# Kernel tuning notes

Measured on AMD Instinct MI355X. Metric: run time of the kernel, lower is better.

The kernel has to match this reference:

```python
import jax, jax.numpy as jnp
import numpy as np

DN = ('NCDHW', 'OIDHW', 'NCDHW')
HEADS, DIM_HEAD = 8, 64
BN_EPS = 1e-5


def conv3d(x, w, stride=1, padding=0, groups=1):
    return jax.lax.conv_general_dilated(
        x, w, window_strides=(stride,) * 3,
        padding=[(padding, padding)] * 3,
        feature_group_count=groups, dimension_numbers=DN)


def batchnorm(x, g, b, m, v):
    sh = (1, -1, 1, 1, 1)
    return (x - m.reshape(sh)) * jax.lax.rsqrt(v.reshape(sh) + BN_EPS) * g.reshape(sh) + b.reshape(sh)


def setup_inputs() -> dict:
    key = jax.random.key(0)
    ks = jax.random.split(key, 6)
    dim, inner = 128, HEADS * DIM_HEAD
    inp = {
        'x': jax.random.normal(ks[0], (4, dim, 16, 16, 16), jnp.float32),
        'wq_dw': jax.random.normal(ks[1], (dim, 1, 3, 3, 3), jnp.float32) * 0.1,
        'bn_q_g': jnp.ones((dim,), jnp.float32),
        'bn_q_b': jnp.zeros((dim,), jnp.float32),
        'bn_q_m': jnp.zeros((dim,), jnp.float32),
        'bn_q_v': jnp.ones((dim,), jnp.float32),
        'wq_pw': jax.random.normal(ks[2], (inner, dim, 1, 1, 1), jnp.float32) * 0.05,
        'wkv_dw': jax.random.normal(ks[3], (dim, 1, 3, 3, 3), jnp.float32) * 0.1,
        'bn_kv_g': jnp.ones((dim,), jnp.float32),
        'bn_kv_b': jnp.zeros((dim,), jnp.float32),
        'bn_kv_m': jnp.zeros((dim,), jnp.float32),
        'bn_kv_v': jnp.ones((dim,), jnp.float32),
        'wkv_pw': jax.random.normal(ks[4], (2 * inner, dim, 1, 1, 1), jnp.float32) * 0.05,
        'w_out': jax.random.normal(ks[5], (dim, inner, 1, 1, 1), jnp.float32) * 0.05,
        'b_out': jnp.zeros((dim,), jnp.float32),
    }
    return inp


def reference(x, wq_dw, bn_q_g, bn_q_b, bn_q_m, bn_q_v, wq_pw,
              wkv_dw, bn_kv_g, bn_kv_b, bn_kv_m, bn_kv_v, wkv_pw,
              w_out, b_out):
    b, c, z, xx, y = x.shape
    h, d = HEADS, DIM_HEAD
    inner = h * d
    scale = d ** -0.5

    # Q projection: depthwise conv (stride 1) -> BN (eval) -> pointwise conv
    q = conv3d(x, wq_dw, stride=1, padding=1, groups=c)
    q = batchnorm(q, bn_q_g, bn_q_b, bn_q_m, bn_q_v)
    q = conv3d(q, wq_pw)                      # [b, inner, z, x, y]

    # KV projection: depthwise conv (stride 2) -> BN -> pointwise conv
    kv = conv3d(x, wkv_dw, stride=2, padding=1, groups=c)
    kv = batchnorm(kv, bn_kv_g, bn_kv_b, bn_kv_m, bn_kv_v)
    kv = conv3d(kv, wkv_pw)                   # [b, 2*inner, z/2, x/2, y/2]
    k, v = kv[:, :inner], kv[:, inner:]

    nq = z * xx * y
    nk = k.shape[2] * k.shape[3] * k.shape[4]
    # channels split as (h d): reshape to [b, h, d, n]
    q4 = q.reshape(b, h, d, nq)
    k4 = k.reshape(b, h, d, nk)
    v4 = v.reshape(b, h, d, nk)

    dots = jnp.einsum('bhdi,bhdj->bhij', q4, k4) * scale   # [b,h,nq,nk]
    attn = jax.nn.softmax(dots, axis=-1)
    out = jnp.einsum('bhij,bhdj->bhdi', attn, v4)          # [b,h,d,nq]
    out = out.reshape(b, inner, z, xx, y)

    out = conv3d(out, w_out) + b_out.reshape(1, -1, 1, 1, 1)
    return out
```

## Files before the change

kernel.cpp:

```cpp
#include <hip/hip_runtime.h>
#include <hip/hip_bf16.h>

typedef __attribute__((ext_vector_type(8))) short short8;
typedef __attribute__((ext_vector_type(4))) short short4v;
typedef __attribute__((ext_vector_type(4))) float f32x4;

#define MFMA16(a, b, c) __builtin_amdgcn_mfma_f32_16x16x32_bf16((a), (b), (c), 0, 0, 0)


__device__ __forceinline__ short f2bf(float f) {
    union { __hip_bfloat16 h; short s; } u;
    u.h = __float2bfloat16(f);
    return u.s;
}

__device__ __forceinline__ unsigned pk2(float lo, float hi) {
    unsigned a = (unsigned short)f2bf(lo);
    unsigned b = (unsigned short)f2bf(hi);
    return a | (b << 16);
}

#define C2SCALE 0.18033688011112042f

__global__ __launch_bounds__(256) void dw_kernel(
    const float* __restrict__ x,
    const float* __restrict__ wq_dw, const float* __restrict__ qg, const float* __restrict__ qb,
    const float* __restrict__ qm, const float* __restrict__ qv,
    const float* __restrict__ wkv_dw, const float* __restrict__ kg, const float* __restrict__ kb,
    const float* __restrict__ km, const float* __restrict__ kv,
    const float* __restrict__ wq_pw, const float* __restrict__ wkv_pw, const float* __restrict__ wo,
    short* __restrict__ qd_t, short* __restrict__ kvd_t,
    short* __restrict__ wq_bf, short* __restrict__ wkv_bf, short* __restrict__ wo_bf) {
    __shared__ float xs[16][3][16][17];
    const int cg = blockIdx.x, by = blockIdx.y, b = blockIdx.z;
    const int tid = threadIdx.x;

    if (by == 24) {
        const int base = (b * 8 + cg) * 256 + tid;
        for (int i = base; i < 65536; i += 8192) {
            int o = i >> 7, cin = i & 127;
            wq_bf[((o >> 4) * 4 + (cin >> 5)) * 512 + (((cin >> 3) & 3) * 16 + (o & 15)) * 8 + (cin & 7)] = f2bf(wq_pw[i]);
        }
        for (int i = base; i < 131072; i += 8192) {
            int o = i >> 7, cin = i & 127;
            wkv_bf[((o >> 4) * 4 + (cin >> 5)) * 512 + (((cin >> 3) & 3) * 16 + (o & 15)) * 8 + (cin & 7)] = f2bf(wkv_pw[i]);
        }
        for (int i = base; i < 65536; i += 8192) {
            int o = i >> 9, cin = i & 511;
            wo_bf[((o >> 4) * 16 + (cin >> 5)) * 512 + (((cin >> 3) & 3) * 16 + (o & 15)) * 8 + (cin & 7)] = f2bf(wo[i]);
        }
        return;
    }

    const int y = tid >> 4, xx = tid & 15;
    const int c0 = cg * 16;

    if (by < 16) {
        const int z = by;
        #pragma unroll 4
        for (int ch = 0; ch < 16; ++ch)
            for (int zz = 0; zz < 3; ++zz) {
                int iz = z + zz - 1;
                float val = 0.f;
                if ((unsigned)iz < 16u)
                    val = x[(((b * 128 + c0 + ch) * 16 + iz) * 16 + y) * 16 + xx];
                xs[ch][zz][y][xx] = val;
            }
        __syncthreads();
        short res[16];
        #pragma unroll
        for (int ch = 0; ch < 16; ++ch) {
            const int c = c0 + ch;
            const float* wc = wq_dw + c * 27;
            float s = 0.f;
            #pragma unroll
            for (int zz = 0; zz < 3; ++zz)
                #pragma unroll
                for (int dy = 0; dy < 3; ++dy) {
                    int iy = y + dy - 1;
                    if ((unsigned)iy < 16u) {
                        float v  = xs[ch][zz][iy][xx];
                        float vm = __shfl_up(v, 1, 16);
                        float vp = __shfl_down(v, 1, 16);
                        float w0 = wc[zz * 9 + dy * 3 + 0];
                        float w1 = wc[zz * 9 + dy * 3 + 1];
                        float w2 = wc[zz * 9 + dy * 3 + 2];
                        if (xx > 0)  s += vm * w0;
                        s += v * w1;
                        if (xx < 15) s += vp * w2;
                    }
                }
            float sc = qg[c] * rsqrtf(qv[c] + 1e-5f);
            float sh = qb[c] - qm[c] * sc;
            res[ch] = f2bf(s * sc + sh);
        }
        const int i = z * 256 + tid;
        const int ib = i >> 4;
        short* dstb = qd_t + (long)b * 524288;
        #pragma unroll
        for (int h2 = 0; h2 < 2; ++h2) {
            short8 ov;
            #pragma unroll
            for (int k = 0; k < 8; ++k) ov[k] = res[h2 * 8 + k];
            *(short8*)(dstb + (ib * 4 + (cg >> 1)) * 512 + (((cg * 2 + h2) & 3) * 16 + xx) * 8) = ov;
        }
    } else {
        const int oz = by - 16;
        #pragma unroll 4
        for (int ch = 0; ch < 16; ++ch)
            for (int zz = 0; zz < 3; ++zz) {
                int iz = 2 * oz + zz - 1;
                float val = 0.f;
                if ((unsigned)iz < 16u)
                    val = x[(((b * 128 + c0 + ch) * 16 + iz) * 16 + y) * 16 + xx];
                xs[ch][zz][y][xx] = val;
            }
        __syncthreads();
        const int pos = tid & 63, cq = tid >> 6;
        const int oy = pos >> 3, ox = pos & 7;
        short4v outv;
        #pragma unroll
        for (int cc = 0; cc < 4; ++cc) {
            const int chl = cq * 4 + cc;
            const int c = c0 + chl;
            const float* wc = wkv_dw + c * 27;
            float s = 0.f;
            #pragma unroll
            for (int zz = 0; zz < 3; ++zz)
                #pragma unroll
                for (int dy = 0; dy < 3; ++dy) {
                    int iy = 2 * oy + dy - 1;
                    if ((unsigned)iy < 16u) {
                        #pragma unroll
                        for (int dx = 0; dx < 3; ++dx) {
                            int ix = 2 * ox + dx - 1;
                            if ((unsigned)ix < 16u)
                                s += xs[chl][zz][iy][ix] * wc[zz * 9 + dy * 3 + dx];
                        }
                    }
                }
            float sc = kg[c] * rsqrtf(kv[c] + 1e-5f);
            float sh = kb[c] - km[c] * sc;
            outv[cc] = f2bf(s * sc + sh);
        }
        const int j = oz * 64 + pos;
        const int jb = j >> 4;
        short* dstb = kvd_t + (long)b * 65536;
        *(short4v*)(dstb + (jb * 4 + (cg >> 1)) * 512 +
                    (((cg * 2 + (cq >> 1)) & 3) * 16 + (j & 15)) * 8 + (cq & 1) * 4) = outv;
    }
}

__global__ __launch_bounds__(256) void pw_kernel(
    const short* __restrict__ wq_bf, const short* __restrict__ wkv_bf,
    const short* __restrict__ qd_t, const short* __restrict__ kvd_t,
    short* __restrict__ q_t, short* __restrict__ k_t, short* __restrict__ v_t) {
    const int xid = blockIdx.x, b = blockIdx.y;
    const int tid = threadIdx.x, lane = tid & 63, wv = tid >> 6;
    const int jl = lane & 15, gq = lane >> 4;
    const int wm = wv >> 1, wn = wv & 1;

    if (xid < 128) {
        const int bi = xid >> 2, bo = xid & 3;
        short8 A[4][4];
        #pragma unroll
        for (int m = 0; m < 4; ++m)
            #pragma unroll
            for (int ks = 0; ks < 4; ++ks)
                A[m][ks] = *(const short8*)(wq_bf + (((bo * 8 + wm * 4 + m) * 4 + ks) * 512) + lane * 8);
        f32x4 acc[4][4];
        #pragma unroll
        for (int m = 0; m < 4; ++m)
            #pragma unroll
            for (int n = 0; n < 4; ++n) acc[m][n] = (f32x4){0.f, 0.f, 0.f, 0.f};
        const short* Bb = qd_t + (long)b * 524288;
        #pragma unroll
        for (int ks = 0; ks < 4; ++ks)
            #pragma unroll
            for (int n = 0; n < 4; ++n) {
                short8 Bf = *(const short8*)(Bb + (((bi * 8 + wn * 4 + n) * 4 + ks) * 512) + lane * 8);
                #pragma unroll
                for (int m = 0; m < 4; ++m) acc[m][n] = MFMA16(A[m][ks], Bf, acc[m][n]);
            }
        const int h = bo * 2 + wm;
        short* qf = q_t + ((long)(b * 8 + h)) * 262144;
        #pragma unroll
        for (int m = 0; m < 4; ++m)
            #pragma unroll
            for (int n = 0; n < 4; ++n) {
                int it = bi * 8 + wn * 4 + n;
                short4v pk;
                #pragma unroll
                for (int r = 0; r < 4; ++r) pk[r] = f2bf(acc[m][n][r] * C2SCALE);
                *(short4v*)(qf + (it * 2 + (m >> 1)) * 512 +
                            (((m & 1) * 2 + (gq >> 1)) * 16 + jl) * 8 + (gq & 1) * 4) = pk;
            }
    } else {
        const int e = xid - 128;
        const int bj = e >> 3, bo = e & 7;
        short8 A[4][4];
        #pragma unroll
        for (int m = 0; m < 4; ++m)
            #pragma unroll
            for (int ks = 0; ks < 4; ++ks)
                A[m][ks] = *(const short8*)(wkv_bf + (((bo * 8 + wm * 4 + m) * 4 + ks) * 512) + lane * 8);
        f32x4 acc[4][4];
        #pragma unroll
        for (int m = 0; m < 4; ++m)
            #pragma unroll
            for (int n = 0; n < 4; ++n) acc[m][n] = (f32x4){0.f, 0.f, 0.f, 0.f};
        const short* Bb = kvd_t + (long)b * 65536;
        #pragma unroll
        for (int ks = 0; ks < 4; ++ks)
            #pragma unroll
            for (int n = 0; n < 4; ++n) {
                short8 Bf = *(const short8*)(Bb + (((bj * 8 + wn * 4 + n) * 4 + ks) * 512) + lane * 8);
                #pragma unroll
                for (int m = 0; m < 4; ++m) acc[m][n] = MFMA16(A[m][ks], Bf, acc[m][n]);
            }
        const int hh = bo * 2 + wm;
        if (hh < 8) {
            short* kf = k_t + ((long)(b * 8 + hh)) * 32768;
            #pragma unroll
            for (int m = 0; m < 4; ++m)
                #pragma unroll
                for (int n = 0; n < 4; ++n) {
                    int jb16 = bj * 8 + wn * 4 + n;
                    short4v pk;
                    #pragma unroll
                    for (int r = 0; r < 4; ++r) pk[r] = f2bf(acc[m][n][r]);
                    *(short4v*)(kf + (jb16 * 2 + (m >> 1)) * 512 +
                                (((m & 1) * 2 + (gq >> 1)) * 16 + jl) * 8 + (gq & 1) * 4) = pk;
                }
        } else {
            short* vf = v_t + ((long)(b * 8 + hh - 8)) * 32768;
            #pragma unroll
            for (int m = 0; m < 4; ++m)
                #pragma unroll
                for (int n = 0; n < 4; ++n) {
                    int frag = ((bj * 4 + wn * 2 + (n >> 1)) * 4 + m);
                    #pragma unroll
                    for (int r = 0; r < 4; ++r)
                        vf[frag * 512 + ((jl >> 2) * 16 + gq * 4 + r) * 8 + (n & 1) * 4 + (jl & 3)]
                            = f2bf(acc[m][n][r]);
                }
        }
    }
}

__global__ __launch_bounds__(256) void attn_kernel(
    const short* __restrict__ q_t, const short* __restrict__ k_t,
    const short* __restrict__ v_t, short* __restrict__ attn_t) {
    const int h = blockIdx.x, b = blockIdx.y, qt = blockIdx.z;
    const int tid = threadIdx.x, lane = tid & 63, wv = tid >> 6;
    const int jl = lane & 15, gq = lane >> 4;
    const long bh = (long)(b * 8 + h);
    const short* qf = q_t + bh * 262144;
    const short* kf = k_t + bh * 32768;
    const short* vf = v_t + bh * 32768;
    const int it0 = qt * 8 + wv * 2;

    short8 QF[2][2];
    #pragma unroll
    for (int t = 0; t < 2; ++t)
        #pragma unroll
        for (int ks = 0; ks < 2; ++ks)
            QF[t][ks] = *(const short8*)(qf + ((it0 + t) * 2 + ks) * 512 + lane * 8);

    f32x4 O[2][4];
    #pragma unroll
    for (int t = 0; t < 2; ++t)
        #pragma unroll
        for (int m = 0; m < 4; ++m) O[t][m] = (f32x4){0.f, 0.f, 0.f, 0.f};
    float l[2] = {0.f, 0.f};

    #pragma unroll 2
    for (int c = 0; c < 8; ++c) {
        f32x4 S[2][4];
        #pragma unroll
        for (int t = 0; t < 2; ++t)
            #pragma unroll
            for (int n = 0; n < 4; ++n) S[t][n] = (f32x4){0.f, 0.f, 0.f, 0.f};
        #pragma unroll
        for (int n = 0; n < 4; ++n)
            #pragma unroll
            for (int ks = 0; ks < 2; ++ks) {
                short8 Kf = *(const short8*)(kf + ((c * 4 + n) * 2 + ks) * 512 + lane * 8);
                S[0][n] = MFMA16(Kf, QF[0][ks], S[0][n]);
                S[1][n] = MFMA16(Kf, QF[1][ks], S[1][n]);
            }
        short8 VV[2][4];
        #pragma unroll
        for (int ks2 = 0; ks2 < 2; ++ks2)
            #pragma unroll
            for (int m = 0; m < 4; ++m)
                VV[ks2][m] = *(const short8*)(vf + ((c * 2 + ks2) * 4 + m) * 512 + lane * 8);
        short8 PW[2][2];
        #pragma unroll
        for (int t = 0; t < 2; ++t) {
            float p[4][4];
            float psum = 0.f;
            #pragma unroll
            for (int n = 0; n < 4; ++n)
                #pragma unroll
                for (int r = 0; r < 4; ++r) {
                    p[n][r] = exp2f(S[t][n][r]);
                    psum += p[n][r];
                }
            l[t] += psum;
            #pragma unroll
            for (int ks2 = 0; ks2 < 2; ++ks2) {
                union { short8 s; unsigned w[4]; } pu;
                pu.w[0] = pk2(p[2 * ks2][0], p[2 * ks2][1]);
                pu.w[1] = pk2(p[2 * ks2][2], p[2 * ks2][3]);
                pu.w[2] = pk2(p[2 * ks2 + 1][0], p[2 * ks2 + 1][1]);
                pu.w[3] = pk2(p[2 * ks2 + 1][2], p[2 * ks2 + 1][3]);
                PW[t][ks2] = pu.s;
            }
        }
        #pragma unroll
        for (int ks2 = 0; ks2 < 2; ++ks2)
            #pragma unroll
            for (int m = 0; m < 4; ++m) {
                O[0][m] = MFMA16(VV[ks2][m], PW[0][ks2], O[0][m]);
                O[1][m] = MFMA16(VV[ks2][m], PW[1][ks2], O[1][m]);
            }
    }
    short* atf = attn_t + (long)b * 2097152;
    #pragma unroll
    for (int t = 0; t < 2; ++t) {
        float lt = l[t];
        lt += __shfl_xor(lt, 16, 64);
        lt += __shfl_xor(lt, 32, 64);
        float inv = 1.f / lt;
        #pragma unroll
        for (int m = 0; m < 4; ++m) {
            short4v pk;
            #pragma unroll
            for (int r = 0; r < 4; ++r) pk[r] = f2bf(O[t][m][r] * inv);
            *(short4v*)(atf + ((it0 + t) * 16 + (h * 2 + (m >> 1))) * 512 +
                        (((m & 1) * 2 + (gq >> 1)) * 16 + jl) * 8 + (gq & 1) * 4) = pk;
        }
    }
}

__global__ __launch_bounds__(256) void out_kernel(
    const short* __restrict__ wo_bf, const short* __restrict__ attn_t,
    const float* __restrict__ bias, float* __restrict__ out) {
    const int bi = blockIdx.x, b = blockIdx.z;
    const int tid = threadIdx.x, lane = tid & 63, wv = tid >> 6;
    const int jl = lane & 15, gq = lane >> 4;
    const int wm = wv >> 1, wn = wv & 1;
    const int o0 = wm * 64;
    const int it16 = bi * 2 + wn;
    f32x4 acc[4];
    #pragma unroll
    for (int m = 0; m < 4; ++m) acc[m] = (f32x4){0.f, 0.f, 0.f, 0.f};
    const short* Bb = attn_t + (long)b * 2097152;
    #pragma unroll 4
    for (int ks = 0; ks < 16; ++ks) {
        short8 Bf = *(const short8*)(Bb + (it16 * 16 + ks) * 512 + lane * 8);
        #pragma unroll
        for (int m = 0; m < 4; ++m) {
            short8 A = *(const short8*)(wo_bf + ((wm * 4 + m) * 16 + ks) * 512 + lane * 8);
            acc[m] = MFMA16(A, Bf, acc[m]);
        }
    }
    const int ii = it16 * 16 + jl;
    #pragma unroll
    for (int m = 0; m < 4; ++m)
        #pragma unroll
        for (int r = 0; r < 4; ++r) {
            int co = o0 + m * 16 + gq * 4 + r;
            out[((long)(b * 128 + co)) * 4096 + ii] = acc[m][r] + bias[co];
        }
}

extern "C" void kernel_launch(void* const* d_in, const int* in_sizes, int n_in,
                              void* d_out, int out_size, void* d_ws, size_t ws_size,
                              hipStream_t stream) {
    const float* x      = (const float*)d_in[0];
    const float* wq_dw  = (const float*)d_in[1];
    const float* bnq_g  = (const float*)d_in[2];
    const float* bnq_b  = (const float*)d_in[3];
    const float* bnq_m  = (const float*)d_in[4];
    const float* bnq_v  = (const float*)d_in[5];
    const float* wq_pw  = (const float*)d_in[6];
    const float* wkv_dw = (const float*)d_in[7];
    const float* bnk_g  = (const float*)d_in[8];
    const float* bnk_b  = (const float*)d_in[9];
    const float* bnk_m  = (const float*)d_in[10];
    const float* bnk_v  = (const float*)d_in[11];
    const float* wkv_pw = (const float*)d_in[12];
    const float* w_out  = (const float*)d_in[13];
    const float* b_out  = (const float*)d_in[14];
    float* out = (float*)d_out;

    char* ws = (char*)d_ws;
    short* wq_bf  = (short*)(ws + 0);
    short* wkv_bf = (short*)(ws + 131072);
    short* wo_bf  = (short*)(ws + 393216);
    short* qd_t   = (short*)(ws + 524288);
    short* kvd_t  = (short*)(ws + 4718592);
    short* q_t    = (short*)(ws + 5242880);
    short* k_t    = (short*)(ws + 22020096);
    short* v_t    = (short*)(ws + 24117248);
    short* attn_t = (short*)(ws + 26214400);

    dw_kernel<<<dim3(8, 25, 4), dim3(256), 0, stream>>>(
        x, wq_dw, bnq_g, bnq_b, bnq_m, bnq_v,
        wkv_dw, bnk_g, bnk_b, bnk_m, bnk_v,
        wq_pw, wkv_pw, w_out,
        qd_t, kvd_t, wq_bf, wkv_bf, wo_bf);
    pw_kernel<<<dim3(160, 4), dim3(256), 0, stream>>>(wq_bf, wkv_bf, qd_t, kvd_t, q_t, k_t, v_t);
    attn_kernel<<<dim3(8, 4, 32), dim3(256), 0, stream>>>(q_t, k_t, v_t, attn_t);
    out_kernel<<<dim3(128, 1, 4), dim3(256), 0, stream>>>(wo_bf, attn_t, b_out, out);
}
```

Baseline: 187.1 us.

## Fuse Q projection, attention and output projection into one kernel

Splits the pointwise stage so only K/V are projected separately, then fuses the Q pointwise projection, softmax-attention over all heads and the output projection into one kernel. Each wave keeps a 16-query tile in registers, loops over heads, and accumulates the output conv directly, so the large q_t and attn_t intermediates never go through global memory. The w_out layout is permuted so the attention output fragments feed MFMA directly. The cost is a much smaller grid (256 blocks), a serial head loop per wave and more register pressure.

```diff
diff --git a/kernel.cpp b/kernel.cpp
--- a/kernel.cpp
+++ b/kernel.cpp
@@ -18,6 +18,15 @@
     unsigned a = (unsigned short)f2bf(lo);
     unsigned b = (unsigned short)f2bf(hi);
     return a | (b << 16);
+}
+
+__device__ __forceinline__ short8 pack8(const f32x4 a, const f32x4 b, float s) {
+    union { short8 v; unsigned w[4]; } u;
+    u.w[0] = pk2(a[0] * s, a[1] * s);
+    u.w[1] = pk2(a[2] * s, a[3] * s);
+    u.w[2] = pk2(b[0] * s, b[1] * s);
+    u.w[3] = pk2(b[2] * s, b[3] * s);
+    return u.v;
 }
 
 #define C2SCALE 0.18033688011112042f
@@ -46,8 +55,11 @@
             wkv_bf[((o >> 4) * 4 + (cin >> 5)) * 512 + (((cin >> 3) & 3) * 16 + (o & 15)) * 8 + (cin & 7)] = f2bf(wkv_pw[i]);
         }
         for (int i = base; i < 65536; i += 8192) {
-            int o = i >> 9, cin = i & 511;
-            wo_bf[((o >> 4) * 16 + (cin >> 5)) * 512 + (((cin >> 3) & 3) * 16 + (o & 15)) * 8 + (cin & 7)] = f2bf(wo[i]);
+            int co = i >> 9, cin = i & 511;
+            int h = cin >> 6, d2 = cin & 63;
+            int m2 = d2 >> 4, gq2 = (d2 >> 2) & 3, r2 = d2 & 3;
+            int frag = ((h * 2 + (m2 >> 1)) * 8 + (co >> 4));
+            wo_bf[frag * 512 + (gq2 * 16 + (co & 15)) * 8 + (m2 & 1) * 4 + r2] = f2bf(wo[i]);
         }
         return;
     }
@@ -151,228 +163,163 @@
     }
 }
 
-__global__ __launch_bounds__(256) void pw_kernel(
-    const short* __restrict__ wq_bf, const short* __restrict__ wkv_bf,
-    const short* __restrict__ qd_t, const short* __restrict__ kvd_t,
-    short* __restrict__ q_t, short* __restrict__ k_t, short* __restrict__ v_t) {
-    const int xid = blockIdx.x, b = blockIdx.y;
+__global__ __launch_bounds__(256) void pwkv_kernel(
+    const short* __restrict__ wkv_bf, const short* __restrict__ kvd_t,
+    short* __restrict__ k_t, short* __restrict__ v_t) {
+    const int e = blockIdx.x, b = blockIdx.y;
+    const int bj = e >> 3, bo = e & 7;
     const int tid = threadIdx.x, lane = tid & 63, wv = tid >> 6;
     const int jl = lane & 15, gq = lane >> 4;
     const int wm = wv >> 1, wn = wv & 1;
-
-    if (xid < 128) {
-        const int bi = xid >> 2, bo = xid & 3;
-        short8 A[4][4];
+    short8 A[4][4];
+    #pragma unroll
+    for (int m = 0; m < 4; ++m)
+        #pragma unroll
+        for (int ks = 0; ks < 4; ++ks)
+            A[m][ks] = *(const short8*)(wkv_bf + (((bo * 8 + wm * 4 + m) * 4 + ks) * 512) + lane * 8);
+    f32x4 acc[4][4];
+    #pragma unroll
+    for (int m = 0; m < 4; ++m)
+        #pragma unroll
+        for (int n = 0; n < 4; ++n) acc[m][n] = (f32x4){0.f, 0.f, 0.f, 0.f};
+    const short* Bb = kvd_t + (long)b * 65536;
+    #pragma unroll
+    for (int ks = 0; ks < 4; ++ks)
+        #pragma unroll
+        for (int n = 0; n < 4; ++n) {
+            short8 Bf = *(const short8*)(Bb + (((bj * 8 + wn * 4 + n) * 4 + ks) * 512) + lane * 8);
+            #pragma unroll
+            for (int m = 0; m < 4; ++m) acc[m][n] = MFMA16(A[m][ks], Bf, acc[m][n]);
+        }
+    const int hh = bo * 2 + wm;
+    if (hh < 8) {
+        short* kf = k_t + ((long)(b * 8 + hh)) * 32768;
         #pragma unroll
         for (int m = 0; m < 4; ++m)
             #pragma unroll
-            for (int ks = 0; ks < 4; ++ks)
-                A[m][ks] = *(const short8*)(wq_bf + (((bo * 8 + wm * 4 + m) * 4 + ks) * 512) + lane * 8);
-        f32x4 acc[4][4];
+            for (int n = 0; n < 4; ++n) {
+                int jt = bj * 8 + wn * 4 + n;
+                short4v pk;
+                #pragma unroll
+                for (int r = 0; r < 4; ++r) pk[r] = f2bf(acc[m][n][r]);
+                *(short4v*)(kf + (jt * 2 + (m >> 1)) * 512 + lane * 8 + (m & 1) * 4) = pk;
+            }
+    } else {
+        short* vf = v_t + ((long)(b * 8 + hh - 8)) * 32768;
         #pragma unroll
         for (int m = 0; m < 4; ++m)
             #pragma unroll
-            for (int n = 0; n < 4; ++n) acc[m][n] = (f32x4){0.f, 0.f, 0.f, 0.f};
-        const short* Bb = qd_t + (long)b * 524288;
-        #pragma unroll
-        for (int ks = 0; ks < 4; ++ks)
-            #pragma unroll
             for (int n = 0; n < 4; ++n) {
-                short8 Bf = *(const short8*)(Bb + (((bi * 8 + wn * 4 + n) * 4 + ks) * 512) + lane * 8);
-                #pragma unroll
-                for (int m = 0; m < 4; ++m) acc[m][n] = MFMA16(A[m][ks], Bf, acc[m][n]);
-            }
-        const int h = bo * 2 + wm;
-        short* qf = q_t + ((long)(b * 8 + h)) * 262144;
-        #pragma unroll
-        for (int m = 0; m < 4; ++m)
-            #pragma unroll
-            for (int n = 0; n < 4; ++n) {
-                int it = bi * 8 + wn * 4 + n;
-                short4v pk;
-                #pragma unroll
-                for (int r = 0; r < 4; ++r) pk[r] = f2bf(acc[m][n][r] * C2SCALE);
-                *(short4v*)(qf + (it * 2 + (m >> 1)) * 512 +
-                            (((m & 1) * 2 + (gq >> 1)) * 16 + jl) * 8 + (gq & 1) * 4) = pk;
-            }
-    } else {
-        const int e = xid - 128;
-        const int bj = e >> 3, bo = e & 7;
-        short8 A[4][4];
-        #pragma unroll
-        for (int m = 0; m < 4; ++m)
-            #pragma unroll
-            for (int ks = 0; ks < 4; ++ks)
-                A[m][ks] = *(const short8*)(wkv_bf + (((bo * 8 + wm * 4 + m) * 4 + ks) * 512) + lane * 8);
-        f32x4 acc[4][4];
-        #pragma unroll
-        for (int m = 0; m < 4; ++m)
-            #pragma unroll
-            for (int n = 0; n < 4; ++n) acc[m][n] = (f32x4){0.f, 0.f, 0.f, 0.f};
-        const short* Bb = kvd_t + (long)b * 65536;
-        #pragma unroll
-        for (int ks = 0; ks < 4; ++ks)
-            #pragma unroll
-            for (int n = 0; n < 4; ++n) {
-                short8 Bf = *(const short8*)(Bb + (((bj * 8 + wn * 4 + n) * 4 + ks) * 512) + lane * 8);
-                #pragma unroll
-                for (int m = 0; m < 4; ++m) acc[m][n] = MFMA16(A[m][ks], Bf, acc[m][n]);
-            }
-        const int hh = bo * 2 + wm;
-        if (hh < 8) {
-            short* kf = k_t + ((long)(b * 8 + hh)) * 32768;
-            #pragma unroll
-            for (int m = 0; m < 4; ++m)
-                #pragma unroll
-                for (int n = 0; n < 4; ++n) {
-                    int jb16 = bj * 8 + wn * 4 + n;
-                    short4v pk;
-                    #pragma unroll
-                    for (int r = 0; r < 4; ++r) pk[r] = f2bf(acc[m][n][r]);
-                    *(short4v*)(kf + (jb16 * 2 + (m >> 1)) * 512 +
-                                (((m & 1) * 2 + (gq >> 1)) * 16 + jl) * 8 + (gq & 1) * 4) = pk;
-                }
-        } else {
-            short* vf = v_t + ((long)(b * 8 + hh - 8)) * 32768;
-            #pragma unroll
-            for (int m = 0; m < 4; ++m)
-                #pragma unroll
-                for (int n = 0; n < 4; ++n) {
-                    int frag = ((bj * 4 + wn * 2 + (n >> 1)) * 4 + m);
-                    #pragma unroll
-                    for (int r = 0; r < 4; ++r)
-                        vf[frag * 512 + ((jl >> 2) * 16 + gq * 4 + r) * 8 + (n & 1) * 4 + (jl & 3)]
-                            = f2bf(acc[m][n][r]);
-                }
-        }
-    }
-}
-
-__global__ __launch_bounds__(256) void attn_kernel(
-    const short* __restrict__ q_t, const short* __restrict__ k_t,
-    const short* __restrict__ v_t, short* __restrict__ attn_t) {
-    const int h = blockIdx.x, b = blockIdx.y, qt = blockIdx.z;
+                int frag = ((bj * 4 + wn * 2 + (n >> 1)) * 4 + m);
+                #pragma unroll
+                for (int r = 0; r < 4; ++r)
+                    vf[frag * 512 + ((jl >> 2) * 16 + gq * 4 + r) * 8 + (n & 1) * 4 + (jl & 3)]
+                        = f2bf(acc[m][n][r]);
+            }
+    }
+}
+
+__global__ __launch_bounds__(256) void fused_kernel(
+    const short* __restrict__ wq_bf, const short* __restrict__ qd_t,
+    const short* __restrict__ k_t, const short* __restrict__ v_t,
+    const short* __restrict__ wo_bf, const float* __restrict__ bias,
+    float* __restrict__ out) {
+    const int rb = blockIdx.x, b = blockIdx.y;
     const int tid = threadIdx.x, lane = tid & 63, wv = tid >> 6;
     const int jl = lane & 15, gq = lane >> 4;
-    const long bh = (long)(b * 8 + h);
-    const short* qf = q_t + bh * 262144;
-    const short* kf = k_t + bh * 32768;
-    const short* vf = v_t + bh * 32768;
-    const int it0 = qt * 8 + wv * 2;
-
-    short8 QF[2][2];
-    #pragma unroll
-    for (int t = 0; t < 2; ++t)
-        #pragma unroll
-        for (int ks = 0; ks < 2; ++ks)
-            QF[t][ks] = *(const short8*)(qf + ((it0 + t) * 2 + ks) * 512 + lane * 8);
-
-    f32x4 O[2][4];
-    #pragma unroll
-    for (int t = 0; t < 2; ++t)
-        #pragma unroll
-        for (int m = 0; m < 4; ++m) O[t][m] = (f32x4){0.f, 0.f, 0.f, 0.f};
-    float l[2] = {0.f, 0.f};
-
-    #pragma unroll 2
-    for (int c = 0; c < 8; ++c) {
-        f32x4 S[2][4];
-        #pragma unroll
-        for (int t = 0; t < 2; ++t)
-            #pragma unroll
-            for (int n = 0; n < 4; ++n) S[t][n] = (f32x4){0.f, 0.f, 0.f, 0.f};
-        #pragma unroll
-        for (int n = 0; n < 4; ++n)
-            #pragma unroll
-            for (int ks = 0; ks < 2; ++ks) {
-                short8 Kf = *(const short8*)(kf + ((c * 4 + n) * 2 + ks) * 512 + lane * 8);
-                S[0][n] = MFMA16(Kf, QF[0][ks], S[0][n]);
-                S[1][n] = MFMA16(Kf, QF[1][ks], S[1][n]);
-            }
-        short8 VV[2][4];
-        #pragma unroll
-        for (int ks2 = 0; ks2 < 2; ++ks2)
-            #pragma unroll
-            for (int m = 0; m < 4; ++m)
-                VV[ks2][m] = *(const short8*)(vf + ((c * 2 + ks2) * 4 + m) * 512 + lane * 8);
-        short8 PW[2][2];
-        #pragma unroll
-        for (int t = 0; t < 2; ++t) {
-            float p[4][4];
-            float psum = 0.f;
+    const int it = rb * 4 + wv;
+
+    short8 qdB[4];
+    {
+        const short* qdb = qd_t + (long)b * 524288;
+        #pragma unroll
+        for (int kc = 0; kc < 4; ++kc)
+            qdB[kc] = *(const short8*)(qdb + (it * 4 + kc) * 512 + lane * 8);
+    }
+
+    f32x4 outacc[8];
+    #pragma unroll
+    for (int o = 0; o < 8; ++o) outacc[o] = (f32x4){0.f, 0.f, 0.f, 0.f};
+
+    #pragma unroll 1
+    for (int h = 0; h < 8; ++h) {
+        const short* kf = k_t + ((long)(b * 8 + h)) * 32768;
+        const short* vf = v_t + ((long)(b * 8 + h)) * 32768;
+        f32x4 qa[4];
+        #pragma unroll
+        for (int ot = 0; ot < 4; ++ot) qa[ot] = (f32x4){0.f, 0.f, 0.f, 0.f};
+        #pragma unroll
+        for (int kc = 0; kc < 4; ++kc)
+            #pragma unroll
+            for (int ot = 0; ot < 4; ++ot) {
+                short8 Af = *(const short8*)(wq_bf + (((h * 4 + ot) * 4 + kc) * 512) + lane * 8);
+                qa[ot] = MFMA16(Af, qdB[kc], qa[ot]);
+            }
+        short8 QB[2];
+        QB[0] = pack8(qa[0], qa[1], C2SCALE);
+        QB[1] = pack8(qa[2], qa[3], C2SCALE);
+
+        f32x4 O[4];
+        #pragma unroll
+        for (int m = 0; m < 4; ++m) O[m] = (f32x4){0.f, 0.f, 0.f, 0.f};
+        float l = 0.f;
+
+        #pragma unroll 2
+        for (int c = 0; c < 8; ++c) {
+            f32x4 S[4];
+            #pragma unroll
+            for (int n = 0; n < 4; ++n) S[n] = (f32x4){0.f, 0.f, 0.f, 0.f};
             #pragma unroll
             for (int n = 0; n < 4; ++n)
                 #pragma unroll
+                for (int ks = 0; ks < 2; ++ks) {
+                    short8 Kf = *(const short8*)(kf + ((c * 4 + n) * 2 + ks) * 512 + lane * 8);
+                    S[n] = MFMA16(Kf, QB[ks], S[n]);
+                }
+            short8 VA[2][4];
+            #pragma unroll
+            for (int ks2 = 0; ks2 < 2; ++ks2)
+                #pragma unroll
+                for (int m = 0; m < 4; ++m)
+                    VA[ks2][m] = *(const short8*)(vf + ((c * 2 + ks2) * 4 + m) * 512 + lane * 8);
+            f32x4 p[4];
+            #pragma unroll
+            for (int n = 0; n < 4; ++n)
+                #pragma unroll
                 for (int r = 0; r < 4; ++r) {
-                    p[n][r] = exp2f(S[t][n][r]);
-                    psum += p[n][r];
+                    p[n][r] = exp2f(S[n][r]);
+                    l += p[n][r];
                 }
-            l[t] += psum;
-            #pragma unroll
-            for (int ks2 = 0; ks2 < 2; ++ks2) {
-                union { short8 s; unsigned w[4]; } pu;
-                pu.w[0] = pk2(p[2 * ks2][0], p[2 * ks2][1]);
-                pu.w[1] = pk2(p[2 * ks2][2], p[2 * ks2][3]);
-                pu.w[2] = pk2(p[2 * ks2 + 1][0], p[2 * ks2 + 1][1]);
-                pu.w[3] = pk2(p[2 * ks2 + 1][2], p[2 * ks2 + 1][3]);
-                PW[t][ks2] = pu.s;
-            }
-        }
-        #pragma unroll
-        for (int ks2 = 0; ks2 < 2; ++ks2)
-            #pragma unroll
-            for (int m = 0; m < 4; ++m) {
-                O[0][m] = MFMA16(VV[ks2][m], PW[0][ks2], O[0][m]);
-                O[1][m] = MFMA16(VV[ks2][m], PW[1][ks2], O[1][m]);
-            }
-    }
-    short* atf = attn_t + (long)b * 2097152;
-    #pragma unroll
-    for (int t = 0; t < 2; ++t) {
-        float lt = l[t];
-        lt += __shfl_xor(lt, 16, 64);
-        lt += __shfl_xor(lt, 32, 64);
-        float inv = 1.f / lt;
-        #pragma unroll
-        for (int m = 0; m < 4; ++m) {
-            short4v pk;
-            #pragma unroll
-            for (int r = 0; r < 4; ++r) pk[r] = f2bf(O[t][m][r] * inv);
-            *(short4v*)(atf + ((it0 + t) * 16 + (h * 2 + (m >> 1))) * 512 +
-                        (((m & 1) * 2 + (gq >> 1)) * 16 + jl) * 8 + (gq & 1) * 4) = pk;
-        }
-    }
-}
-
-__global__ __launch_bounds__(256) void out_kernel(
-    const short* __restrict__ wo_bf, const short* __restrict__ attn_t,
-    const float* __restrict__ bias, float* __restrict__ out) {
-    const int bi = blockIdx.x, b = blockIdx.z;
-    const int tid = threadIdx.x, lane = tid & 63, wv = tid >> 6;
-    const int jl = lane & 15, gq = lane >> 4;
-    const int wm = wv >> 1, wn = wv & 1;
-    const int o0 = wm * 64;
-    const int it16 = bi * 2 + wn;
-    f32x4 acc[4];
-    #pragma unroll
-    for (int m = 0; m < 4; ++m) acc[m] = (f32x4){0.f, 0.f, 0.f, 0.f};
-    const short* Bb = attn_t + (long)b * 2097152;
-    #pragma unroll 4
-    for (int ks = 0; ks < 16; ++ks) {
-        short8 Bf = *(const short8*)(Bb + (it16 * 16 + ks) * 512 + lane * 8);
-        #pragma unroll
-        for (int m = 0; m < 4; ++m) {
-            short8 A = *(const short8*)(wo_bf + ((wm * 4 + m) * 16 + ks) * 512 + lane * 8);
-            acc[m] = MFMA16(A, Bf, acc[m]);
-        }
-    }
-    const int ii = it16 * 16 + jl;
-    #pragma unroll
-    for (int m = 0; m < 4; ++m)
+            short8 PW[2];
+            PW[0] = pack8(p[0], p[1], 1.f);
+            PW[1] = pack8(p[2], p[3], 1.f);
+            #pragma unroll
+            for (int ks2 = 0; ks2 < 2; ++ks2)
+                #pragma unroll
+                for (int m = 0; m < 4; ++m)
+                    O[m] = MFMA16(VA[ks2][m], PW[ks2], O[m]);
+        }
+        l += __shfl_xor(l, 16, 64);
+        l += __shfl_xor(l, 32, 64);
+        float inv = 1.f / l;
+        short8 PB[2];
+        PB[0] = pack8(O[0], O[1], inv);
+        PB[1] = pack8(O[2], O[3], inv);
+        #pragma unroll
+        for (int ks3 = 0; ks3 < 2; ++ks3)
+            #pragma unroll
+            for (int ot2 = 0; ot2 < 8; ++ot2) {
+                short8 Wf = *(const short8*)(wo_bf + (((h * 2 + ks3) * 8 + ot2) * 512) + lane * 8);
+                outacc[ot2] = MFMA16(Wf, PB[ks3], outacc[ot2]);
+            }
+    }
+    const int ii = it * 16 + jl;
+    #pragma unroll
+    for (int ot2 = 0; ot2 < 8; ++ot2)
         #pragma unroll
         for (int r = 0; r < 4; ++r) {
-            int co = o0 + m * 16 + gq * 4 + r;
-            out[((long)(b * 128 + co)) * 4096 + ii] = acc[m][r] + bias[co];
+            int co = ot2 * 16 + gq * 4 + r;
+            out[((long)(b * 128 + co)) * 4096 + ii] = outacc[ot2][r] + bias[co];
         }
 }
 
@@ -402,17 +349,14 @@
     short* wo_bf  = (short*)(ws + 393216);
     short* qd_t   = (short*)(ws + 524288);
     short* kvd_t  = (short*)(ws + 4718592);
-    short* q_t    = (short*)(ws + 5242880);
-    short* k_t    = (short*)(ws + 22020096);
-    short* v_t    = (short*)(ws + 24117248);
-    short* attn_t = (short*)(ws + 26214400);
+    short* k_t    = (short*)(ws + 5242880);
+    short* v_t    = (short*)(ws + 7340032);
 
     dw_kernel<<<dim3(8, 25, 4), dim3(256), 0, stream>>>(
         x, wq_dw, bnq_g, bnq_b, bnq_m, bnq_v,
         wkv_dw, bnk_g, bnk_b, bnk_m, bnk_v,
         wq_pw, wkv_pw, w_out,
         qd_t, kvd_t, wq_bf, wkv_bf, wo_bf);
-    pw_kernel<<<dim3(160, 4), dim3(256), 0, stream>>>(wq_bf, wkv_bf, qd_t, kvd_t, q_t, k_t, v_t);
-    attn_kernel<<<dim3(8, 4, 32), dim3(256), 0, stream>>>(q_t, k_t, v_t, attn_t);
-    out_kernel<<<dim3(128, 1, 4), dim3(256), 0, stream>>>(wo_bf, attn_t, b_out, out);
-}
+    pwkv_kernel<<<dim3(32, 4), dim3(256), 0, stream>>>(wkv_bf, kvd_t, k_t, v_t);
+    fused_kernel<<<dim3(64, 4), dim3(256), 0, stream>>>(wq_bf, qd_t, k_t, v_t, wo_bf, b_out, out);
+}
```

After: 229.3 us. 22.5% more time.
